# Kernel optimization log

Hardware: AMD Instinct MI355X
Metric: run time of the kernel (lower is better)

The kernel has to match this reference:

```python
import jax, jax.numpy as jnp
import numpy as np

N_QUBITS = 4
N_LAYERS = 2
BATCH = 1048576


def _rx(theta):
    # PennyLane RX(theta) = exp(-i theta X / 2)
    c = jnp.cos(theta / 2).astype(jnp.complex64)
    s = jnp.sin(theta / 2).astype(jnp.complex64)
    return jnp.stack([jnp.stack([c, -1j * s]), jnp.stack([-1j * s, c])])


def _rot(phi, theta, omega):
    # PennyLane Rot(phi, theta, omega) = RZ(omega) RY(theta) RZ(phi)
    ct = jnp.cos(theta / 2)
    st = jnp.sin(theta / 2)
    e1 = jnp.exp(-0.5j * (phi + omega))
    e2 = jnp.exp(0.5j * (phi - omega))
    e3 = jnp.exp(-0.5j * (phi - omega))
    e4 = jnp.exp(0.5j * (phi + omega))
    return jnp.stack([jnp.stack([e1 * ct, -e2 * st]),
                      jnp.stack([e3 * st, e4 * ct])]).astype(jnp.complex64)


def _apply_1q(psi, U, w):
    # psi: (2,)*N_QUBITS complex statevector; contract U on wire w
    psi = jnp.tensordot(U, psi, axes=([1], [w]))
    return jnp.moveaxis(psi, 0, w)


def _apply_cnot(psi, c, t):
    psi = jnp.moveaxis(psi, (c, t), (0, 1))
    psi = jnp.stack([psi[0], psi[1, ::-1]], axis=0)  # flip target where control=1
    return jnp.moveaxis(psi, (0, 1), (c, t))


def _circuit(x, weights):
    psi = jnp.zeros((2,) * N_QUBITS, jnp.complex64).at[(0,) * N_QUBITS].set(1.0)
    # AngleEmbedding: RX(x[i]) on each wire
    for w in range(N_QUBITS):
        psi = _apply_1q(psi, _rx(x[w]), w)
    # StronglyEntanglingLayers: Rot per wire, then CNOT ring with range r
    for l in range(N_LAYERS):
        for w in range(N_QUBITS):
            psi = _apply_1q(psi, _rot(weights[l, w, 0], weights[l, w, 1], weights[l, w, 2]), w)
        r = (l % (N_QUBITS - 1)) + 1  # default ranges in StronglyEntanglingLayers
        for w in range(N_QUBITS):
            psi = _apply_cnot(psi, w, (w + r) % N_QUBITS)
    probs = jnp.real(psi * jnp.conj(psi))
    sign = jnp.array([1.0, -1.0], jnp.float32)
    z = [jnp.sum(probs * sign.reshape([2 if a == i else 1 for a in range(N_QUBITS)]))
         for i in range(N_QUBITS)]
    return jnp.stack(z)  # <Z_i> for each wire, shape [4]


def setup_inputs() -> dict:
    key = jax.random.key(0)
    k1, k2, k3, k4 = jax.random.split(key, 4)
    noise = jax.random.normal(k1, (BATCH, N_QUBITS), dtype=jnp.float32)
    q_weights = jax.random.normal(k2, (N_LAYERS, N_QUBITS, 3), dtype=jnp.float32) * 0.1
    W = jax.random.normal(k3, (4, N_QUBITS), dtype=jnp.float32) * 0.5
    b = jax.random.normal(k4, (4,), dtype=jnp.float32) * 0.1
    return {"noise": noise, "q_weights": q_weights, "W": W, "b": b}


def reference(noise, q_weights, W, b):
    q_out = jax.vmap(lambda x: _circuit(x, q_weights))(noise)  # [B, 4] float32
    out = q_out @ W.T + b                                      # Linear(4, 4)
    energy = jnp.abs(out[:, 0]) + 0.001
    return jnp.concatenate([energy[:, None], out[:, 1:]], axis=1)
```

## Files before the change

### kernel.cpp

```cpp
#include <hip/hip_runtime.h>
#include <math.h>


__global__ __launch_bounds__(256) void qg_precompute(
    const float* __restrict__ qw,
    const float* __restrict__ Wm,
    const float* __restrict__ bv,
    float* __restrict__ Dcoef)
{
  __shared__ float  gm[24][8];
  __shared__ float2 Ul[16][16];
  __shared__ float  wj[4][16];
  __shared__ float2 A[4][16][16];
  const int tid = threadIdx.x;

  if (tid < 24) {
    const float phi = qw[tid*3 + 0];
    const float th  = qw[tid*3 + 1];
    const float om  = qw[tid*3 + 2];
    float st, ct, sa, ca, sd, cd;
    __sincosf(0.5f*th,       &st, &ct);
    __sincosf(0.5f*(phi+om), &sa, &ca);
    __sincosf(0.5f*(phi-om), &sd, &cd);
    gm[tid][0] =  ca*ct; gm[tid][1] = -sa*ct;
    gm[tid][2] = -cd*st; gm[tid][3] = -sd*st;
    gm[tid][4] =  cd*st; gm[tid][5] = -sd*st;
    gm[tid][6] =  ca*ct; gm[tid][7] =  sa*ct;
  }
  if (tid >= 192) {
    const int j = (tid - 192) >> 4, k = tid & 15;
    float s = 0.f;
    #pragma unroll
    for (int i = 0; i < 4; ++i)
      s += Wm[j*4 + i] * (((k >> (3 - i)) & 1) ? -1.f : 1.f);
    wj[j][k] = s;
  }
  __syncthreads();

  {
    const int col = tid >> 4, row = tid & 15;
    float vr = (row == col) ? 1.f : 0.f, vi = 0.f;
    #pragma unroll
    for (int l = 0; l < 2; ++l) {
      #pragma unroll
      for (int w = 0; w < 4; ++w) {
        const int g = l*4 + w;
        const float m00r = gm[g][0], m00i = gm[g][1];
        const float m01r = gm[g][2], m01i = gm[g][3];
        const float m10r = gm[g][4], m10i = gm[g][5];
        const float m11r = gm[g][6], m11i = gm[g][7];
        const int mask = 8 >> w;
        const float pr = __shfl_xor(vr, mask);
        const float pi = __shfl_xor(vi, mask);
        float nr, ni;
        if (!(row & mask)) {
          nr = m00r*vr - m00i*vi + m01r*pr - m01i*pi;
          ni = m00r*vi + m00i*vr + m01r*pi + m01i*pr;
        } else {
          nr = m10r*pr - m10i*pi + m11r*vr - m11i*vi;
          ni = m10r*pi + m10i*pr + m11r*vi + m11i*vr;
        }
        vr = nr; vi = ni;
      }
      const int r = l + 1;
      #pragma unroll
      for (int w = 0; w < 4; ++w) {
        const int t  = (w + r) & 3;
        const int cm = 8 >> w, tm = 8 >> t;
        const float pr = __shfl_xor(vr, tm);
        const float pi = __shfl_xor(vi, tm);
        if (row & cm) { vr = pr; vi = pi; }
      }
    }
    Ul[row][col] = make_float2(vr, vi);
  }
  __syncthreads();

  {
    const int s = tid >> 4, t = tid & 15;
    float ar[4] = {0,0,0,0}, ai[4] = {0,0,0,0};
    #pragma unroll
    for (int k = 0; k < 16; ++k) {
      const float2 us = Ul[k][s], ut = Ul[k][t];
      const float pr = us.x*ut.x + us.y*ut.y;
      const float pi = us.x*ut.y - us.y*ut.x;
      #pragma unroll
      for (int j = 0; j < 4; ++j) { ar[j] += wj[j][k]*pr; ai[j] += wj[j][k]*pi; }
    }
    #pragma unroll
    for (int j = 0; j < 4; ++j) A[j][s][t] = make_float2(ar[j], ai[j]);
  }
  __syncthreads();

  for (int item = tid; item < 324; item += 256) {
    const int j = item / 81, p = item % 81;
    const int p1 = p / 27, p2 = (p / 9) % 3, p3 = (p / 3) % 3, p4 = p % 3;
    int ym = 0, ny = 0;
    if (p1 == 2) { ym |= 8; ++ny; }
    if (p2 == 2) { ym |= 4; ++ny; }
    if (p3 == 2) { ym |= 2; ++ny; }
    if (p4 == 2) { ym |= 1; ++ny; }
    float sum = 0.f;
    for (int t = 0; t < 16; ++t) {
      const int t0 = (t>>3)&1, t1 = (t>>2)&1, t2 = (t>>1)&1, t3 = t&1;
      float sgn = 1.f;
      if      (p1 == 1) sgn *= t0 ? -1.f : 1.f;
      else if (p1 == 2) sgn *= t0 ?  1.f : -1.f;
      if      (p2 == 1) sgn *= t1 ? -1.f : 1.f;
      else if (p2 == 2) sgn *= t1 ?  1.f : -1.f;
      if      (p3 == 1) sgn *= t2 ? -1.f : 1.f;
      else if (p3 == 2) sgn *= t2 ?  1.f : -1.f;
      if      (p4 == 1) sgn *= t3 ? -1.f : 1.f;
      else if (p4 == 2) sgn *= t3 ?  1.f : -1.f;
      const float2 ae = A[j][t ^ ym][t];
      const int m = ny & 3;
      const float re = (m == 0) ? ae.x : (m == 1) ? -ae.y : (m == 2) ? -ae.x : ae.y;
      sum += sgn * re;
    }
    sum *= 0.0625f;
    if (p == 0) sum += bv[j];
    Dcoef[item] = sum;
  }
}

#define Q0  v0.x
#define Q1  v0.y
#define Q2  v0.z
#define Q3  v0.w
#define Q4  v1.x
#define Q5  v1.y
#define Q6  v1.z
#define Q7  v1.w
#define Q8  v2.x
#define Q9  v2.y
#define Q10 v2.z
#define Q11 v2.w
#define Q12 v3.x
#define Q13 v3.y
#define Q14 v3.z
#define Q15 v3.w
#define Q16 v4.x
#define Q17 v4.y
#define Q18 v4.z
#define Q19 v4.w
#define Q20 v5.x
#define Q21 v5.y
#define Q22 v5.z
#define Q23 v5.w
#define Q24 v6.x
#define Q25 v6.y
#define Q26 v6.z
#define Q27 v6.w
#define Q28 v7.x
#define Q29 v7.y
#define Q30 v7.z
#define Q31 v7.w
#define Q32 v8.x
#define Q33 v8.y
#define Q34 v8.z
#define Q35 v8.w
#define Q36 v9.x
#define Q37 v9.y
#define Q38 v9.z
#define Q39 v9.w
#define Q40 v10.x
#define Q41 v10.y
#define Q42 v10.z
#define Q43 v10.w
#define Q44 v11.x
#define Q45 v11.y
#define Q46 v11.z
#define Q47 v11.w
#define Q48 v12.x
#define Q49 v12.y
#define Q50 v12.z
#define Q51 v12.w
#define Q52 v13.x
#define Q53 v13.y
#define Q54 v13.z
#define Q55 v13.w
#define Q56 v14.x
#define Q57 v14.y
#define Q58 v14.z
#define Q59 v14.w
#define Q60 v15.x
#define Q61 v15.y
#define Q62 v15.z
#define Q63 v15.w
#define Q64 v16.x
#define Q65 v16.y
#define Q66 v16.z
#define Q67 v16.w
#define Q68 v17.x
#define Q69 v17.y
#define Q70 v17.z
#define Q71 v17.w
#define Q72 v18.x
#define Q73 v18.y
#define Q74 v18.z
#define Q75 v18.w
#define Q76 v19.x
#define Q77 v19.y
#define Q78 v19.z
#define Q79 v19.w
#define Q80 q80

__global__ __launch_bounds__(256, 4) void qg_main(
    const float4* __restrict__ noise,
    const float*  __restrict__ Dg,
    float4* __restrict__ out,
    int B)
{
  __shared__ float tbl[4*84];
  __shared__ float tr[256][5];

  const int tid  = threadIdx.x;
  const int wv   = tid >> 6;
  const int lane = tid & 63;

  for (int i = tid; i < 324; i += 256) {
    const int j = i / 81, p = i - j*81;
    tbl[j*84 + p] = Dg[i];
  }
  __syncthreads();

  const float4* Tj = (const float4*)&tbl[wv * 84];
  const float4 v0  = Tj[0],  v1  = Tj[1],  v2  = Tj[2],  v3  = Tj[3];
  const float4 v4  = Tj[4],  v5  = Tj[5],  v6  = Tj[6],  v7  = Tj[7];
  const float4 v8  = Tj[8],  v9  = Tj[9],  v10 = Tj[10], v11 = Tj[11];
  const float4 v12 = Tj[12], v13 = Tj[13], v14 = Tj[14], v15 = Tj[15];
  const float4 v16 = Tj[16], v17 = Tj[17], v18 = Tj[18], v19 = Tj[19];
  const float q80  = tbl[wv * 84 + 80];

  const int Bm1 = B - 1;

  int base = blockIdx.x * 512;
  #pragma unroll
  for (int it = 0; it < 2; ++it, base += 256) {
    #pragma unroll
    for (int s = 0; s < 4; ++s) {
      const int e = base + s*64 + lane;
      const float4 x = noise[min(e, Bm1)];
      float s0,c0,s1,c1,s2,c2,s3,c3;
      __sincosf(x.x, &s0, &c0);
      __sincosf(x.y, &s1, &c1);
      __sincosf(x.z, &s2, &c2);
      __sincosf(x.w, &s3, &c3);

      const float g34_1 =  c3,     g34_2 = -s3,
                  g34_3 =  c2,     g34_4 =  c2*c3,  g34_5 = -c2*s3,
                  g34_6 = -s2,     g34_7 = -s2*c3,  g34_8 =  s2*s3;
      const float g12_1 =  c1,     g12_2 = -s1,
                  g12_3 =  c0,     g12_4 =  c0*c1,  g12_5 = -c0*s1,
                  g12_6 = -s0,     g12_7 = -s0*c1,  g12_8 =  s0*s1;

      float acc, h;
#define ABLK(A0,A1,A2,A3,A4,A5,A6,A7,A8) {      \
      h = A0;                                   \
      h = fmaf(A1, g34_1, h);                   \
      h = fmaf(A2, g34_2, h);                   \
      h = fmaf(A3, g34_3, h);                   \
      h = fmaf(A4, g34_4, h);                   \
      h = fmaf(A5, g34_5, h);                   \
      h = fmaf(A6, g34_6, h);                   \
      h = fmaf(A7, g34_7, h);                   \
      h = fmaf(A8, g34_8, h); }

      ABLK(Q0, Q1, Q2, Q3, Q4, Q5, Q6, Q7, Q8)          acc = h;
      ABLK(Q9, Q10,Q11,Q12,Q13,Q14,Q15,Q16,Q17)         acc = fmaf(g12_1, h, acc);
      ABLK(Q18,Q19,Q20,Q21,Q22,Q23,Q24,Q25,Q26)         acc = fmaf(g12_2, h, acc);
      ABLK(Q27,Q28,Q29,Q30,Q31,Q32,Q33,Q34,Q35)         acc = fmaf(g12_3, h, acc);
      ABLK(Q36,Q37,Q38,Q39,Q40,Q41,Q42,Q43,Q44)         acc = fmaf(g12_4, h, acc);
      ABLK(Q45,Q46,Q47,Q48,Q49,Q50,Q51,Q52,Q53)         acc = fmaf(g12_5, h, acc);
      ABLK(Q54,Q55,Q56,Q57,Q58,Q59,Q60,Q61,Q62)         acc = fmaf(g12_6, h, acc);
      ABLK(Q63,Q64,Q65,Q66,Q67,Q68,Q69,Q70,Q71)         acc = fmaf(g12_7, h, acc);
      ABLK(Q72,Q73,Q74,Q75,Q76,Q77,Q78,Q79,Q80)         acc = fmaf(g12_8, h, acc);
#undef ABLK

      if (wv == 0) acc = fabsf(acc) + 0.001f;
      tr[s*64 + lane][wv] = acc;
    }
    __syncthreads();
    {
      const int e = base + tid;
      const float o0 = tr[tid][0], o1 = tr[tid][1];
      const float o2 = tr[tid][2], o3 = tr[tid][3];
      if (e < B) out[e] = make_float4(o0, o1, o2, o3);
    }
    __syncthreads();
  }
}

extern "C" void kernel_launch(void* const* d_in, const int* in_sizes, int n_in,
                              void* d_out, int out_size, void* d_ws, size_t ws_size,
                              hipStream_t stream) {
  const float* noise = (const float*)d_in[0];
  const float* qw    = (const float*)d_in[1];
  const float* Wm    = (const float*)d_in[2];
  const float* bv    = (const float*)d_in[3];
  float* Dcoef = (float*)d_ws;
  const int B = in_sizes[0] / 4;

  hipLaunchKernelGGL(qg_precompute, dim3(1), dim3(256), 0, stream, qw, Wm, bv, Dcoef);

  const int blocks = (B + 511) / 512;
  hipLaunchKernelGGL(qg_main, dim3(blocks), dim3(256), 0, stream,
                     (const float4*)noise, (const float*)Dcoef, (float4*)d_out, B);
}
```

Baseline: 27.60 us.

## Fuse coefficient precompute into main kernel, recomputing per block

Drops the single-block precompute kernel and its workspace round trip. Every block of the main kernel now builds the 81-term coefficient table itself in shared memory before processing its batch slice. This removes one launch and the serial dependency between the two kernels, but repeats the small precompute (sincos, 16x16 complex matmuls) in each of about 2048 blocks. It also raises shared-memory use and lowers the occupancy hint from 4 to 3. The sincos calls are split into separate __sinf/__cosf calls.

```diff
diff --git a/kernel.cpp b/kernel.cpp
--- a/kernel.cpp
+++ b/kernel.cpp
@@ -2,26 +2,29 @@
 #include <math.h>
 
 
-__global__ __launch_bounds__(256) void qg_precompute(
-    const float* __restrict__ qw,
-    const float* __restrict__ Wm,
-    const float* __restrict__ bv,
-    float* __restrict__ Dcoef)
+__global__ __launch_bounds__(256, 3) void qg_fused(
+    const float4* __restrict__ noise,
+    const float*  __restrict__ qw,
+    const float*  __restrict__ Wm,
+    const float*  __restrict__ bv,
+    float4* __restrict__ out,
+    int B)
 {
   __shared__ float  gm[24][8];
   __shared__ float2 Ul[16][16];
   __shared__ float  wj[4][16];
   __shared__ float2 A[4][16][16];
+  __shared__ float  tbl[4*84];
+  __shared__ float  tr[256][5];
   const int tid = threadIdx.x;
 
   if (tid < 24) {
     const float phi = qw[tid*3 + 0];
     const float th  = qw[tid*3 + 1];
     const float om  = qw[tid*3 + 2];
-    float st, ct, sa, ca, sd, cd;
-    __sincosf(0.5f*th,       &st, &ct);
-    __sincosf(0.5f*(phi+om), &sa, &ca);
-    __sincosf(0.5f*(phi-om), &sd, &cd);
+    const float st = __sinf(0.5f*th),       ct = __cosf(0.5f*th);
+    const float sa = __sinf(0.5f*(phi+om)), ca = __cosf(0.5f*(phi+om));
+    const float sd = __sinf(0.5f*(phi-om)), cd = __cosf(0.5f*(phi-om));
     gm[tid][0] =  ca*ct; gm[tid][1] = -sa*ct;
     gm[tid][2] = -cd*st; gm[tid][3] = -sd*st;
     gm[tid][4] =  cd*st; gm[tid][5] = -sd*st;
@@ -119,9 +122,12 @@
     }
     sum *= 0.0625f;
     if (p == 0) sum += bv[j];
-    Dcoef[item] = sum;
-  }
-}
+    tbl[j*84 + p] = sum;
+  }
+  __syncthreads();
+
+  const int wv   = tid >> 6;
+  const int lane = tid & 63;
 
 #define Q0  v0.x
 #define Q1  v0.y
@@ -205,25 +211,6 @@
 #define Q79 v19.w
 #define Q80 q80
 
-__global__ __launch_bounds__(256, 4) void qg_main(
-    const float4* __restrict__ noise,
-    const float*  __restrict__ Dg,
-    float4* __restrict__ out,
-    int B)
-{
-  __shared__ float tbl[4*84];
-  __shared__ float tr[256][5];
-
-  const int tid  = threadIdx.x;
-  const int wv   = tid >> 6;
-  const int lane = tid & 63;
-
-  for (int i = tid; i < 324; i += 256) {
-    const int j = i / 81, p = i - j*81;
-    tbl[j*84 + p] = Dg[i];
-  }
-  __syncthreads();
-
   const float4* Tj = (const float4*)&tbl[wv * 84];
   const float4 v0  = Tj[0],  v1  = Tj[1],  v2  = Tj[2],  v3  = Tj[3];
   const float4 v4  = Tj[4],  v5  = Tj[5],  v6  = Tj[6],  v7  = Tj[7];
@@ -241,11 +228,10 @@
     for (int s = 0; s < 4; ++s) {
       const int e = base + s*64 + lane;
       const float4 x = noise[min(e, Bm1)];
-      float s0,c0,s1,c1,s2,c2,s3,c3;
-      __sincosf(x.x, &s0, &c0);
-      __sincosf(x.y, &s1, &c1);
-      __sincosf(x.z, &s2, &c2);
-      __sincosf(x.w, &s3, &c3);
+      const float s0 = __sinf(x.x), c0 = __cosf(x.x);
+      const float s1 = __sinf(x.y), c1 = __cosf(x.y);
+      const float s2 = __sinf(x.z), c2 = __cosf(x.z);
+      const float s3 = __sinf(x.w), c3 = __cosf(x.w);
 
       const float g34_1 =  c3,     g34_2 = -s3,
                   g34_3 =  c2,     g34_4 =  c2*c3,  g34_5 = -c2*s3,
@@ -298,12 +284,9 @@
   const float* qw    = (const float*)d_in[1];
   const float* Wm    = (const float*)d_in[2];
   const float* bv    = (const float*)d_in[3];
-  float* Dcoef = (float*)d_ws;
   const int B = in_sizes[0] / 4;
 
-  hipLaunchKernelGGL(qg_precompute, dim3(1), dim3(256), 0, stream, qw, Wm, bv, Dcoef);
-
   const int blocks = (B + 511) / 512;
-  hipLaunchKernelGGL(qg_main, dim3(blocks), dim3(256), 0, stream,
-                     (const float4*)noise, (const float*)Dcoef, (float4*)d_out, B);
+  hipLaunchKernelGGL(qg_fused, dim3(blocks), dim3(256), 0, stream,
+                     (const float4*)noise, qw, Wm, bv, (float4*)d_out, B);
 }
```

Result: slower. 34.27 us (+24.2%).
